# Kernel optimization log

Measured on AMD Instinct MI355X. Metric: run time of the kernel, lower is better.

## Reference

```python
import jax, jax.numpy as jnp
import numpy as np

G = 1.0 / 7.0  # grid cell size


def _iou(a, b):
    # a, b: tuples (x1, y1, x2, y2) of broadcastable arrays
    ix1 = jnp.maximum(a[0], b[0])
    iy1 = jnp.maximum(a[1], b[1])
    ix2 = jnp.minimum(a[2], b[2])
    iy2 = jnp.minimum(a[3], b[3])
    inter = jnp.clip(ix2 - ix1, 0.0) * jnp.clip(iy2 - iy1, 0.0)
    area_a = (a[2] - a[0]) * (a[3] - a[1])
    area_b = (b[2] - b[0]) * (b[3] - b[1])
    union = area_a + area_b - inter
    return inter / jnp.where(union == 0.0, 1.0, union)


def setup_inputs() -> dict:
    key = jax.random.key(0)
    k1, k2, k3 = jax.random.split(key, 3)
    B = 8192
    pred = jax.random.uniform(k1, (B, 30, 7, 7), jnp.float32, 0.05, 0.95)
    label = jax.random.uniform(k2, (B, 30, 7, 7), jnp.float32, 0.05, 0.95)
    # channel 4 of label is the objectness indicator, exactly 0 or 1
    obj = (jax.random.uniform(k3, (B, 7, 7)) < 0.3).astype(jnp.float32)
    label = label.at[:, 4].set(obj)
    return {"pred": pred, "label": label}


def _yolo_loss(pred, label, noobj_weight=0.5):
    obj_weight = 1.0 - noobj_weight
    B = pred.shape[0]
    # i indexes axis 2 (paired with x), j indexes axis 3 (paired with y)
    ii = jnp.arange(7, dtype=pred.dtype).reshape(7, 1)
    jj = jnp.arange(7, dtype=pred.dtype).reshape(1, 7)

    def mk_box(x, y, w, h):
        cx = (x + ii) * G
        cy = (y + jj) * G
        return (cx - w / 2, cy - h / 2, cx + w / 2, cy + h / 2)

    b1 = mk_box(pred[:, 0], pred[:, 1], pred[:, 2], pred[:, 3])
    b2 = mk_box(pred[:, 5], pred[:, 6], pred[:, 7], pred[:, 8])
    # label box exactly as in the source (degenerate: x2==x1, y2==y1)
    lx = (label[:, 0] + ii) * G - label[:, 2] / 2
    ly = (label[:, 1] + jj) * G - label[:, 3] / 2
    bl = (lx, ly, lx, ly)

    iou1 = _iou(b1, bl)
    iou2 = _iou(b2, bl)
    sel1 = iou1 > iou2            # (B,7,7): box 1 is responsible
    obj = label[:, 4] == 1.0      # (B,7,7)

    # per-cell coordinate terms for each box
    t1 = (jnp.sum((pred[:, 0:2] - label[:, 0:2]) ** 2, axis=1)
          + jnp.sum((jnp.sqrt(pred[:, 2:4]) - jnp.sqrt(label[:, 2:4])) ** 2, axis=1))
    t2 = (jnp.sum((pred[:, 5:7] - label[:, 5:7]) ** 2, axis=1)
          + jnp.sum((jnp.sqrt(pred[:, 7:9]) - jnp.sqrt(label[:, 7:9])) ** 2, axis=1))
    obj_term = jnp.where(sel1, t1, t2)
    conf_term = jnp.where(sel1, (pred[:, 4] - 1.0) ** 2, (pred[:, 9] - 1.0) ** 2)
    noobj_obj_term = jnp.where(sel1, pred[:, 9] ** 2, pred[:, 4] ** 2)
    noobj_empty_term = pred[:, 4] ** 2 + pred[:, 9] ** 2
    cls_term = jnp.sum((pred[:, 10:] - label[:, 10:]) ** 2, axis=1)

    zero = jnp.zeros((), pred.dtype)
    obj_loss = jnp.sum(jnp.where(obj, obj_term, zero))
    confidence_loss = jnp.sum(jnp.where(obj, conf_term, zero))
    classes_loss = jnp.sum(jnp.where(obj, cls_term, zero))
    noobj_loss = jnp.sum(jnp.where(obj, noobj_obj_term, noobj_empty_term))

    return (obj_loss * obj_weight + noobj_loss * noobj_weight
            + classes_loss + confidence_loss) / B


def reference(pred, label):
    return _yolo_loss(pred, label, noobj_weight=0.5)
```

## Files before the change

### kernel.cpp

```cpp
#include <hip/hip_runtime.h>


constexpr int NT = 512;
constexpr int NB = 512;

__device__ __forceinline__ float sq(float x) { return x * x; }

__global__ __launch_bounds__(NT) void yolo_loss_kernel(
    const float* __restrict__ pred, const float* __restrict__ label,
    float* __restrict__ out, int ncells, float inv_B)
{
    const float Gc = 1.0f / 7.0f;
    float acc = 0.0f;

    for (int g = blockIdx.x * NT + threadIdx.x; g < ncells; g += NB * NT) {
        int b = g / 49;
        int s = g - b * 49;
        int i = s / 7;
        int j = s - i * 7;
        const float* __restrict__ P = pred  + (size_t)b * 1470 + s;
        const float* __restrict__ L = label + (size_t)b * 1470 + s;

        float p[30], l[30];
#pragma unroll
        for (int c = 0; c < 30; ++c) {
            p[c] = P[c * 49];
            l[c] = L[c * 49];
        }

        float fi = (float)i, fj = (float)j;

        float cx1 = (p[0] + fi) * Gc, cy1 = (p[1] + fj) * Gc;
        float a_x1 = cx1 - p[2] * 0.5f, a_y1 = cy1 - p[3] * 0.5f;
        float a_x2 = cx1 + p[2] * 0.5f, a_y2 = cy1 + p[3] * 0.5f;
        float cx2 = (p[5] + fi) * Gc, cy2 = (p[6] + fj) * Gc;
        float b_x1 = cx2 - p[7] * 0.5f, b_y1 = cy2 - p[8] * 0.5f;
        float b_x2 = cx2 + p[7] * 0.5f, b_y2 = cy2 + p[8] * 0.5f;
        float lx = (l[0] + fi) * Gc - l[2] * 0.5f;
        float ly = (l[1] + fj) * Gc - l[3] * 0.5f;

        auto iou_pt = [&](float x1, float y1, float x2, float y2) {
            float ix = fminf(x2, lx) - fmaxf(x1, lx);
            float iy = fminf(y2, ly) - fmaxf(y1, ly);
            float inter = fmaxf(ix, 0.0f) * fmaxf(iy, 0.0f);
            float area_a = (x2 - x1) * (y2 - y1);
            float uni = area_a + 0.0f - inter;
            float denom = (uni == 0.0f) ? 1.0f : uni;
            return inter / denom;
        };

        float iou1 = iou_pt(a_x1, a_y1, a_x2, a_y2);
        float iou2 = iou_pt(b_x1, b_y1, b_x2, b_y2);
        bool sel1 = iou1 > iou2;

        float t1 = sq(p[0] - l[0]) + sq(p[1] - l[1])
                 + sq(sqrtf(p[2]) - sqrtf(l[2])) + sq(sqrtf(p[3]) - sqrtf(l[3]));
        float t2 = sq(p[5] - l[5]) + sq(p[6] - l[6])
                 + sq(sqrtf(p[7]) - sqrtf(l[7])) + sq(sqrtf(p[8]) - sqrtf(l[8]));

        float obj_term     = sel1 ? t1 : t2;
        float conf_term    = sel1 ? sq(p[4] - 1.0f) : sq(p[9] - 1.0f);
        float noobj_obj    = sel1 ? sq(p[9]) : sq(p[4]);
        float noobj_empty  = sq(p[4]) + sq(p[9]);

        float cls = 0.0f;
#pragma unroll
        for (int c = 10; c < 30; ++c) cls += sq(p[c] - l[c]);

        bool obj = (l[4] == 1.0f);
        acc += obj ? (0.5f * obj_term + conf_term + cls + 0.5f * noobj_obj)
                   : (0.5f * noobj_empty);
    }

#pragma unroll
    for (int off = 32; off > 0; off >>= 1)
        acc += __shfl_down(acc, off, 64);

    __shared__ float swave[NT / 64];
    int lane = threadIdx.x & 63;
    int wid  = threadIdx.x >> 6;
    if (lane == 0) swave[wid] = acc;
    __syncthreads();
    if (threadIdx.x == 0) {
        float bs = 0.0f;
#pragma unroll
        for (int w = 0; w < NT / 64; ++w) bs += swave[w];
        atomicAdd(out, bs * inv_B);
    }
}

extern "C" void kernel_launch(void* const* d_in, const int* in_sizes, int n_in,
                              void* d_out, int out_size, void* d_ws, size_t ws_size,
                              hipStream_t stream) {
    const float* pred  = (const float*)d_in[0];
    const float* label = (const float*)d_in[1];
    float* out = (float*)d_out;

    int B = in_sizes[0] / 1470;
    int ncells = B * 49;

    hipMemsetAsync(d_out, 0, sizeof(float), stream);

    yolo_loss_kernel<<<NB, NT, 0, stream>>>(pred, label, out, ncells,
                                            1.0f / (float)B);
}
```

Baseline: 114.9 us.

## Stage per-block batch items into LDS via direct global-to-LDS loads

Each block now handles 4 batch items. It copies their full pred and label tensors into shared memory using 16-byte global_load_lds instructions, then computes per-cell terms by reading from LDS. The old grid-stride loop issued strided 4-byte global loads (stride 49 floats). The new copy is contiguous and vectorized, and the grid grows to one block per 4 items. In exchange it uses about 47KB of LDS per block, which limits occupancy, and adds a barrier with one-shot load-then-compute with no overlap across items.

```diff
diff --git a/kernel.cpp b/kernel.cpp
--- a/kernel.cpp
+++ b/kernel.cpp
@@ -1,25 +1,65 @@
 #include <hip/hip_runtime.h>
+#include <stdint.h>
 
 
-constexpr int NT = 512;
-constexpr int NB = 512;
+constexpr int NT    = 256;
+constexpr int ITEMS = 4;
+constexpr int FL_PER_ITEM = 1470;
+constexpr int NF4   = ITEMS * FL_PER_ITEM / 4;
+constexpr int NROUND = (NF4 + NT - 1) / NT;
+constexpr int NF4_PAD = NROUND * NT;
 
 __device__ __forceinline__ float sq(float x) { return x * x; }
 
+__device__ __forceinline__ void g2lds16(const void* g, void* l) {
+    __builtin_amdgcn_global_load_lds(
+        (const __attribute__((address_space(1))) void*)g,
+        (__attribute__((address_space(3))) void*)l,
+        16, 0, 0);
+}
+
 __global__ __launch_bounds__(NT) void yolo_loss_kernel(
     const float* __restrict__ pred, const float* __restrict__ label,
-    float* __restrict__ out, int ncells, float inv_B)
+    float* __restrict__ out, int B, float inv_B)
 {
+    __shared__ float sp[NF4_PAD * 4];
+    __shared__ float sl[NF4_PAD * 4];
+    __shared__ float swave[NT / 64];
+
+    const int tid = threadIdx.x;
+    const int b0  = blockIdx.x * ITEMS;
+    const int items = min(ITEMS, B - b0);
+
+    if (items == ITEMS) {
+        const char* pg = (const char*)pred  + (size_t)b0 * (FL_PER_ITEM * 4);
+        const char* lg = (const char*)label + (size_t)b0 * (FL_PER_ITEM * 4);
+#pragma unroll
+        for (int k = 0; k < NROUND; ++k) {
+            int t  = k * NT + tid;
+            int tc = t < NF4 ? t : NF4 - 1;
+            g2lds16(pg + (size_t)tc * 16, (char*)sp + (size_t)t * 16);
+            g2lds16(lg + (size_t)tc * 16, (char*)sl + (size_t)t * 16);
+        }
+    } else {
+        const float* pg = pred  + (size_t)b0 * FL_PER_ITEM;
+        const float* lg = label + (size_t)b0 * FL_PER_ITEM;
+        for (int t = tid; t < items * FL_PER_ITEM; t += NT) {
+            sp[t] = pg[t];
+            sl[t] = lg[t];
+        }
+    }
+    __syncthreads();
+
     const float Gc = 1.0f / 7.0f;
     float acc = 0.0f;
 
-    for (int g = blockIdx.x * NT + threadIdx.x; g < ncells; g += NB * NT) {
-        int b = g / 49;
-        int s = g - b * 49;
+    for (int t = tid; t < items * 49; t += NT) {
+        int k = t / 49;
+        int s = t - k * 49;
         int i = s / 7;
         int j = s - i * 7;
-        const float* __restrict__ P = pred  + (size_t)b * 1470 + s;
-        const float* __restrict__ L = label + (size_t)b * 1470 + s;
+        const float* P = sp + k * FL_PER_ITEM + s;
+        const float* L = sl + k * FL_PER_ITEM + s;
 
         float p[30], l[30];
 #pragma unroll
@@ -76,7 +116,6 @@
     for (int off = 32; off > 0; off >>= 1)
         acc += __shfl_down(acc, off, 64);
 
-    __shared__ float swave[NT / 64];
     int lane = threadIdx.x & 63;
     int wid  = threadIdx.x >> 6;
     if (lane == 0) swave[wid] = acc;
@@ -97,10 +136,10 @@
     float* out = (float*)d_out;
 
     int B = in_sizes[0] / 1470;
-    int ncells = B * 49;
+    int NB = (B + ITEMS - 1) / ITEMS;
 
     hipMemsetAsync(d_out, 0, sizeof(float), stream);
 
-    yolo_loss_kernel<<<NB, NT, 0, stream>>>(pred, label, out, ncells,
+    yolo_loss_kernel<<<NB, NT, 0, stream>>>(pred, label, out, B,
                                             1.0f / (float)B);
 }
```

Result: slower. 123.3 us (+7.3%).
